# Kernel tuning notes

Hardware: AMD Instinct MI355X
Metric: run time of the kernel (lower is better)

Reference implementation:

```python
import jax, jax.numpy as jnp
import numpy as np

WINDOW = 9
REG_WEIGHT = 1.0


def _box_filter(x, k):
    """Sum over a k^3 box via three separable 1D ones-convs (== conv3d with ones kernel)."""
    pad = k // 2
    for ax in range(3):  # D, H, W spatial axes
        kshape = [1, 1, 1, 1, 1]
        kshape[2 + ax] = k
        kern = jnp.ones(kshape, x.dtype)
        padding = [(pad, pad) if i == ax else (0, 0) for i in range(3)]
        x = jax.lax.conv_general_dilated(
            x, kern, window_strides=(1, 1, 1), padding=padding,
            dimension_numbers=("NCDHW", "OIDHW", "NCDHW"))
    return x


def _ncc_loss(pred, target, k):
    win_size = jnp.asarray(float(k ** 3), pred.dtype)
    pred_sum = _box_filter(pred, k)
    target_sum = _box_filter(target, k)
    pred_sq_sum = _box_filter(pred * pred, k)
    target_sq_sum = _box_filter(target * target, k)
    pred_target_sum = _box_filter(pred * target, k)
    pred_mean = pred_sum / win_size
    target_mean = target_sum / win_size
    cross = (pred_target_sum - target_mean * pred_sum - pred_mean * target_sum
             + pred_mean * target_mean * win_size)
    pred_var = pred_sq_sum - 2.0 * pred_mean * pred_sum + pred_mean * pred_mean * win_size
    target_var = target_sq_sum - 2.0 * target_mean * target_sum + target_mean * target_mean * win_size
    pred_var = jnp.clip(pred_var, 0.0, None)
    target_var = jnp.clip(target_var, 0.0, None)
    cc = cross * cross / (pred_var * target_var + 0.001)
    cc = jnp.clip(cc, 0.0, 1.0)
    return 1.0 - jnp.mean(cc)


def _gradient_loss(flow):
    dy = jnp.abs(flow[:, :, 1:, :, :] - flow[:, :, :-1, :, :])
    dx = jnp.abs(flow[:, :, :, 1:, :] - flow[:, :, :, :-1, :])
    dz = jnp.abs(flow[:, :, :, :, 1:] - flow[:, :, :, :, :-1])
    return (jnp.mean(dy) + jnp.mean(dx) + jnp.mean(dz)) / 3.0


def setup_inputs() -> dict:
    key = jax.random.key(0)
    k1, k2, k3 = jax.random.split(key, 3)
    B, D, H, W = 2, 160, 160, 160
    moved = jax.random.uniform(k1, (B, 1, D, H, W), dtype=jnp.float32)
    fixed = jax.random.uniform(k2, (B, 1, D, H, W), dtype=jnp.float32)
    flow = jax.random.normal(k3, (B, 3, D, H, W), dtype=jnp.float32)
    return {"moved": moved, "fixed": fixed, "flow": flow}


def reference(moved, fixed, flow):
    sim_loss = _ncc_loss(moved, fixed, WINDOW)
    reg_loss = _gradient_loss(flow)
    total_loss = sim_loss + REG_WEIGHT * reg_loss
    return total_loss
```

## Files before the change

### kernel.cpp

```cpp
#include <hip/hip_runtime.h>

#define DD 160
#define HH 160
#define WW 160
#define VOL (DD * HH * WW)
#define PLANE (HH * WW)
#define NB 2
#define HT 16
#define HS (HT + 8)
#define LDW 164
#define DCH 20
#define NDCH (DD / DCH)
#define CPT 50
#define DREDBLK (CPT * NDCH)
#define GCHD 20
#define GBLK (NB * 3 * (DD / GCHD) * HH * (WW / 4) / 256)

typedef _Float16 h4 __attribute__((ext_vector_type(4)));
typedef _Float16 h2 __attribute__((ext_vector_type(2)));

__global__ __launch_bounds__(512, 4) void ncc_wh(const float* __restrict__ mv,
                                                 const float* __restrict__ fx,
                                                 _Float16* __restrict__ out) {
    __shared__ float wsum[5][HS][LDW];

    const int d   = blockIdx.y;
    const int b   = blockIdx.z;
    const int h0  = blockIdx.x * HT;
    const int tid = threadIdx.x;

    if (tid < 480) {
        const int r  = tid / 20;
        const int s  = tid - r * 20;
        const int h  = h0 - 4 + r;
        const int w0 = 8 * s;

        float vm[16], vf[16];
#pragma unroll
        for (int i = 0; i < 16; ++i) { vm[i] = 0.f; vf[i] = 0.f; }

        if ((unsigned)h < (unsigned)HH) {
            const float* rowm = mv + (size_t)b * VOL + ((size_t)d * HH + h) * WW;
            const float* rowf = fx + (size_t)b * VOL + ((size_t)d * HH + h) * WW;
#pragma unroll
            for (int j = 0; j < 4; ++j) {
                const int w4 = w0 - 4 + 4 * j;
                if (w4 >= 0 && w4 <= WW - 4) {
                    float4 m4 = *(const float4*)(rowm + w4);
                    float4 f4 = *(const float4*)(rowf + w4);
                    vm[4*j+0] = m4.x; vm[4*j+1] = m4.y; vm[4*j+2] = m4.z; vm[4*j+3] = m4.w;
                    vf[4*j+0] = f4.x; vf[4*j+1] = f4.y; vf[4*j+2] = f4.z; vf[4*j+3] = f4.w;
                } else {
#pragma unroll
                    for (int e = 0; e < 4; ++e) {
                        const int w = w4 + e;
                        if ((unsigned)w < (unsigned)WW) {
                            vm[4*j+e] = rowm[w];
                            vf[4*j+e] = rowf[w];
                        }
                    }
                }
            }
        }

        float o0[8], o1[8], o2[8], o3[8], o4[8];
        float sm = 0.f, sf = 0.f, smm = 0.f, sff = 0.f, smf = 0.f;
#pragma unroll
        for (int i = 0; i < 9; ++i) {
            float m = vm[i], f = vf[i];
            sm += m; sf += f;
            smm = fmaf(m, m, smm);
            sff = fmaf(f, f, sff);
            smf = fmaf(m, f, smf);
        }
        o0[0] = sm; o1[0] = sf; o2[0] = smm; o3[0] = sff; o4[0] = smf;
#pragma unroll
        for (int k = 1; k < 8; ++k) {
            float am = vm[k + 8], bm = vm[k - 1];
            float af = vf[k + 8], bf = vf[k - 1];
            sm  += am - bm;
            sf  += af - bf;
            smm += fmaf(am, am, -(bm * bm));
            sff += fmaf(af, af, -(bf * bf));
            smf += fmaf(am, af, -(bm * bf));
            o0[k] = sm; o1[k] = sf; o2[k] = smm; o3[k] = sff; o4[k] = smf;
        }
        *(float4*)&wsum[0][r][w0]     = *(float4*)&o0[0];
        *(float4*)&wsum[0][r][w0 + 4] = *(float4*)&o0[4];
        *(float4*)&wsum[1][r][w0]     = *(float4*)&o1[0];
        *(float4*)&wsum[1][r][w0 + 4] = *(float4*)&o1[4];
        *(float4*)&wsum[2][r][w0]     = *(float4*)&o2[0];
        *(float4*)&wsum[2][r][w0 + 4] = *(float4*)&o2[4];
        *(float4*)&wsum[3][r][w0]     = *(float4*)&o3[0];
        *(float4*)&wsum[3][r][w0 + 4] = *(float4*)&o3[4];
        *(float4*)&wsum[4][r][w0]     = *(float4*)&o4[0];
        *(float4*)&wsum[4][r][w0 + 4] = *(float4*)&o4[4];
    }
    __syncthreads();

    if (tid < 400) {
        const int f    = tid / 80;
        const int rem  = tid - f * 80;
        const int half = rem / 40;
        const int w    = 4 * (rem - half * 40);
        const int ro0  = 8 * half;

        float4 s9 = make_float4(0.f, 0.f, 0.f, 0.f);
#pragma unroll
        for (int t = 0; t < 9; ++t) {
            float4 v = *(const float4*)&wsum[f][ro0 + t][w];
            s9.x += v.x; s9.y += v.y; s9.z += v.z; s9.w += v.w;
        }
        _Float16* ob = out + (size_t)(b * 5 + f) * VOL
                           + ((size_t)d * HH + h0 + ro0) * WW + w;
        h4 o;
        o.x = (_Float16)s9.x; o.y = (_Float16)s9.y;
        o.z = (_Float16)s9.z; o.w = (_Float16)s9.w;
        *(h4*)ob = o;
#pragma unroll
        for (int ro = 1; ro < 8; ++ro) {
            float4 aa = *(const float4*)&wsum[f][ro0 + ro + 8][w];
            float4 bb = *(const float4*)&wsum[f][ro0 + ro - 1][w];
            s9.x += aa.x - bb.x; s9.y += aa.y - bb.y;
            s9.z += aa.z - bb.z; s9.w += aa.w - bb.w;
            o.x = (_Float16)s9.x; o.y = (_Float16)s9.y;
            o.z = (_Float16)s9.z; o.w = (_Float16)s9.w;
            *(h4*)(ob + (size_t)ro * WW) = o;
        }
    }
}

__global__ __launch_bounds__(256) void ncc_dred(const _Float16* __restrict__ fields,
                                                float* __restrict__ partial) {
    const int hw = (blockIdx.x * 256 + threadIdx.x) * 2;
    const int d0 = blockIdx.y * DCH;
    const _Float16* p0 = fields + (size_t)blockIdx.z * 5 * VOL + hw;

    float s0a = 0.f, s1a = 0.f, s2a = 0.f, s3a = 0.f, s4a = 0.f;
    float s0b = 0.f, s1b = 0.f, s2b = 0.f, s3b = 0.f, s4b = 0.f;
    {
        int lo = d0 - 4 > 0 ? d0 - 4 : 0;
        int hi = d0 + 4 < DD - 1 ? d0 + 4 : DD - 1;
        for (int dd = lo; dd <= hi; ++dd) {
            const _Float16* p = p0 + (size_t)dd * PLANE;
            h2 v0 = *(const h2*)(p + 0 * (size_t)VOL);
            h2 v1 = *(const h2*)(p + 1 * (size_t)VOL);
            h2 v2 = *(const h2*)(p + 2 * (size_t)VOL);
            h2 v3 = *(const h2*)(p + 3 * (size_t)VOL);
            h2 v4 = *(const h2*)(p + 4 * (size_t)VOL);
            s0a += (float)v0.x; s0b += (float)v0.y;
            s1a += (float)v1.x; s1b += (float)v1.y;
            s2a += (float)v2.x; s2b += (float)v2.y;
            s3a += (float)v3.x; s3b += (float)v3.y;
            s4a += (float)v4.x; s4b += (float)v4.y;
        }
    }

    float acc = 0.f;
    const float inv_win = 1.0f / 729.0f;
    for (int d = d0; d < d0 + DCH; ++d) {
        {
            float cross = fmaf(-(s0a * s1a), inv_win, s4a);
            float pv = fmaxf(fmaf(-(s0a * s0a), inv_win, s2a), 0.f);
            float tv = fmaxf(fmaf(-(s1a * s1a), inv_win, s3a), 0.f);
            float cc = cross * cross / (pv * tv + 0.001f);
            acc += fminf(fmaxf(cc, 0.f), 1.f);
        }
        {
            float cross = fmaf(-(s0b * s1b), inv_win, s4b);
            float pv = fmaxf(fmaf(-(s0b * s0b), inv_win, s2b), 0.f);
            float tv = fmaxf(fmaf(-(s1b * s1b), inv_win, s3b), 0.f);
            float cc = cross * cross / (pv * tv + 0.001f);
            acc += fminf(fmaxf(cc, 0.f), 1.f);
        }

        if (d + 1 < d0 + DCH) {
            if (d + 5 < DD) {
                const _Float16* p = p0 + (size_t)(d + 5) * PLANE;
                h2 v0 = *(const h2*)(p + 0 * (size_t)VOL);
                h2 v1 = *(const h2*)(p + 1 * (size_t)VOL);
                h2 v2 = *(const h2*)(p + 2 * (size_t)VOL);
                h2 v3 = *(const h2*)(p + 3 * (size_t)VOL);
                h2 v4 = *(const h2*)(p + 4 * (size_t)VOL);
                s0a += (float)v0.x; s0b += (float)v0.y;
                s1a += (float)v1.x; s1b += (float)v1.y;
                s2a += (float)v2.x; s2b += (float)v2.y;
                s3a += (float)v3.x; s3b += (float)v3.y;
                s4a += (float)v4.x; s4b += (float)v4.y;
            }
            if (d - 4 >= 0) {
                const _Float16* p = p0 + (size_t)(d - 4) * PLANE;
                h2 v0 = *(const h2*)(p + 0 * (size_t)VOL);
                h2 v1 = *(const h2*)(p + 1 * (size_t)VOL);
                h2 v2 = *(const h2*)(p + 2 * (size_t)VOL);
                h2 v3 = *(const h2*)(p + 3 * (size_t)VOL);
                h2 v4 = *(const h2*)(p + 4 * (size_t)VOL);
                s0a -= (float)v0.x; s0b -= (float)v0.y;
                s1a -= (float)v1.x; s1b -= (float)v1.y;
                s2a -= (float)v2.x; s2b -= (float)v2.y;
                s3a -= (float)v3.x; s3b -= (float)v3.y;
                s4a -= (float)v4.x; s4b -= (float)v4.y;
            }
        }
    }

    for (int o = 32; o > 0; o >>= 1) acc += __shfl_down(acc, o, 64);
    __shared__ float red[4];
    int lane = threadIdx.x & 63, wid = threadIdx.x >> 6;
    if (lane == 0) red[wid] = acc;
    __syncthreads();
    if (threadIdx.x == 0)
        partial[((size_t)blockIdx.z * NDCH + blockIdx.y) * CPT + blockIdx.x] =
            red[0] + red[1] + red[2] + red[3];
}

__global__ __launch_bounds__(256) void grad_red(const float* __restrict__ fl,
                                                float* __restrict__ partial) {
    const int gid = blockIdx.x * 256 + threadIdx.x;
    const int w4  = gid % 40;
    int t = gid / 40;
    const int h  = t % HH;  t /= HH;
    const int dc = t % (DD / GCHD); t /= (DD / GCHD);
    const int bc = t;
    const int d0 = dc * GCHD;
    const int w  = w4 * 4;

    const float* base = fl + (size_t)bc * VOL;
    float acc = 0.f;
    float4 v = *(const float4*)(base + ((size_t)d0 * HH + h) * WW + w);
    for (int d = d0; d < d0 + GCHD; ++d) {
        const float* pd = base + ((size_t)d * HH + h) * WW + w;
        float4 vn = v;
        if (d < DD - 1) {
            vn = *(const float4*)(pd + PLANE);
            acc += fabsf(vn.x - v.x) + fabsf(vn.y - v.y) +
                   fabsf(vn.z - v.z) + fabsf(vn.w - v.w);
        }
        if (h < HH - 1) {
            float4 vh = *(const float4*)(pd + WW);
            acc += fabsf(vh.x - v.x) + fabsf(vh.y - v.y) +
                   fabsf(vh.z - v.z) + fabsf(vh.w - v.w);
        }
        acc += fabsf(v.y - v.x) + fabsf(v.z - v.y) + fabsf(v.w - v.z);
        if (w < WW - 4) acc += fabsf(pd[4] - v.w);
        v = vn;
    }

    for (int o = 32; o > 0; o >>= 1) acc += __shfl_down(acc, o, 64);
    __shared__ float red[4];
    int lane = threadIdx.x & 63, wid = threadIdx.x >> 6;
    if (lane == 0) red[wid] = acc;
    __syncthreads();
    if (threadIdx.x == 0) partial[blockIdx.x] = red[0] + red[1] + red[2] + red[3];
}

__global__ __launch_bounds__(256) void finalize(const float* __restrict__ pcc, int ncc,
                                                const float* __restrict__ pg, int ng,
                                                float* __restrict__ out) {
    __shared__ float red[4];
    int lane = threadIdx.x & 63, wid = threadIdx.x >> 6;

    float a = 0.f;
    for (int i = threadIdx.x; i < ncc; i += 256) a += pcc[i];
    for (int o = 32; o > 0; o >>= 1) a += __shfl_down(a, o, 64);
    if (lane == 0) red[wid] = a;
    __syncthreads();
    float asum = red[0] + red[1] + red[2] + red[3];
    __syncthreads();

    float g = 0.f;
    for (int i = threadIdx.x; i < ng; i += 256) g += pg[i];
    for (int o = 32; o > 0; o >>= 1) g += __shfl_down(g, o, 64);
    if (lane == 0) red[wid] = g;
    __syncthreads();
    float gsum = red[0] + red[1] + red[2] + red[3];

    if (threadIdx.x == 0) {
        float sim = 1.0f - asum / 8192000.0f;
        float reg = gsum / 73267200.0f;
        out[0] = sim + reg;
    }
}

extern "C" void kernel_launch(void* const* d_in, const int* in_sizes, int n_in,
                              void* d_out, int out_size, void* d_ws, size_t ws_size,
                              hipStream_t stream) {
    const float* moved  = (const float*)d_in[0];
    const float* fixedp = (const float*)d_in[1];
    const float* flow   = (const float*)d_in[2];
    float* out = (float*)d_out;

    _Float16* fields = (_Float16*)d_ws;
    float* pcc = (float*)(fields + (size_t)NB * 5 * VOL);
    float* pg  = pcc + NB * DREDBLK;

    grad_red<<<GBLK, 256, 0, stream>>>(flow, pg);
    ncc_wh<<<dim3(HH / HT, DD, NB), 512, 0, stream>>>(moved, fixedp, fields);
    ncc_dred<<<dim3(CPT, NDCH, NB), 256, 0, stream>>>(fields, pcc);
    finalize<<<1, 256, 0, stream>>>(pcc, NB * DREDBLK, pg, GBLK, out);
}
```

Baseline: 97.65 us.

## Store W-pass sums as fp16 in LDS, widen H-pass to 8 columns, halve D chunk

The intermediate W-direction window sums in shared memory are now stored as fp16 instead of fp32, halving LDS footprint so occupancy can rise (launch bound min blocks raised to 6). The H-pass threads now process 8 columns by 4 rows with 16-byte fp16 loads and stores instead of 4 columns by 8 rows. The D-reduction chunk size is halved, doubling blocks in that kernel. Rounding intermediate sums to fp16 before the H sum adds precision loss, especially for squared sums.

```diff
diff --git a/kernel.cpp b/kernel.cpp
--- a/kernel.cpp
+++ b/kernel.cpp
@@ -8,21 +8,21 @@
 #define NB 2
 #define HT 16
 #define HS (HT + 8)
-#define LDW 164
-#define DCH 20
+#define LDWH 168
+#define DCH 10
 #define NDCH (DD / DCH)
 #define CPT 50
 #define DREDBLK (CPT * NDCH)
 #define GCHD 20
 #define GBLK (NB * 3 * (DD / GCHD) * HH * (WW / 4) / 256)
 
-typedef _Float16 h4 __attribute__((ext_vector_type(4)));
+typedef _Float16 h8 __attribute__((ext_vector_type(8)));
 typedef _Float16 h2 __attribute__((ext_vector_type(2)));
 
-__global__ __launch_bounds__(512, 4) void ncc_wh(const float* __restrict__ mv,
+__global__ __launch_bounds__(512, 6) void ncc_wh(const float* __restrict__ mv,
                                                  const float* __restrict__ fx,
                                                  _Float16* __restrict__ out) {
-    __shared__ float wsum[5][HS][LDW];
+    __shared__ _Float16 wsum[5][HS][LDWH];
 
     const int d   = blockIdx.y;
     const int b   = blockIdx.z;
@@ -85,47 +85,48 @@
             smf += fmaf(am, af, -(bm * bf));
             o0[k] = sm; o1[k] = sf; o2[k] = smm; o3[k] = sff; o4[k] = smf;
         }
-        *(float4*)&wsum[0][r][w0]     = *(float4*)&o0[0];
-        *(float4*)&wsum[0][r][w0 + 4] = *(float4*)&o0[4];
-        *(float4*)&wsum[1][r][w0]     = *(float4*)&o1[0];
-        *(float4*)&wsum[1][r][w0 + 4] = *(float4*)&o1[4];
-        *(float4*)&wsum[2][r][w0]     = *(float4*)&o2[0];
-        *(float4*)&wsum[2][r][w0 + 4] = *(float4*)&o2[4];
-        *(float4*)&wsum[3][r][w0]     = *(float4*)&o3[0];
-        *(float4*)&wsum[3][r][w0 + 4] = *(float4*)&o3[4];
-        *(float4*)&wsum[4][r][w0]     = *(float4*)&o4[0];
-        *(float4*)&wsum[4][r][w0 + 4] = *(float4*)&o4[4];
+#define PACK_STORE(fi, arr) {                                   \
+            h8 t_;                                              \
+            _Pragma("unroll")                                   \
+            for (int j_ = 0; j_ < 8; ++j_) t_[j_] = (_Float16)arr[j_]; \
+            *(h8*)&wsum[fi][r][w0] = t_; }
+        PACK_STORE(0, o0) PACK_STORE(1, o1) PACK_STORE(2, o2)
+        PACK_STORE(3, o3) PACK_STORE(4, o4)
+#undef PACK_STORE
     }
     __syncthreads();
 
     if (tid < 400) {
-        const int f    = tid / 80;
-        const int rem  = tid - f * 80;
-        const int half = rem / 40;
-        const int w    = 4 * (rem - half * 40);
-        const int ro0  = 8 * half;
-
-        float4 s9 = make_float4(0.f, 0.f, 0.f, 0.f);
+        const int f   = tid / 80;
+        const int rem = tid - f * 80;
+        const int q   = rem / 20;
+        const int w   = 8 * (rem - q * 20);
+        const int ro0 = 4 * q;
+
+        float sa[8];
+#pragma unroll
+        for (int j = 0; j < 8; ++j) sa[j] = 0.f;
 #pragma unroll
         for (int t = 0; t < 9; ++t) {
-            float4 v = *(const float4*)&wsum[f][ro0 + t][w];
-            s9.x += v.x; s9.y += v.y; s9.z += v.z; s9.w += v.w;
+            h8 v = *(const h8*)&wsum[f][ro0 + t][w];
+#pragma unroll
+            for (int j = 0; j < 8; ++j) sa[j] += (float)v[j];
         }
         _Float16* ob = out + (size_t)(b * 5 + f) * VOL
                            + ((size_t)d * HH + h0 + ro0) * WW + w;
-        h4 o;
-        o.x = (_Float16)s9.x; o.y = (_Float16)s9.y;
-        o.z = (_Float16)s9.z; o.w = (_Float16)s9.w;
-        *(h4*)ob = o;
-#pragma unroll
-        for (int ro = 1; ro < 8; ++ro) {
-            float4 aa = *(const float4*)&wsum[f][ro0 + ro + 8][w];
-            float4 bb = *(const float4*)&wsum[f][ro0 + ro - 1][w];
-            s9.x += aa.x - bb.x; s9.y += aa.y - bb.y;
-            s9.z += aa.z - bb.z; s9.w += aa.w - bb.w;
-            o.x = (_Float16)s9.x; o.y = (_Float16)s9.y;
-            o.z = (_Float16)s9.z; o.w = (_Float16)s9.w;
-            *(h4*)(ob + (size_t)ro * WW) = o;
+        h8 o;
+#pragma unroll
+        for (int j = 0; j < 8; ++j) o[j] = (_Float16)sa[j];
+        *(h8*)ob = o;
+#pragma unroll
+        for (int ro = 1; ro < 4; ++ro) {
+            h8 va = *(const h8*)&wsum[f][ro0 + ro + 8][w];
+            h8 vb = *(const h8*)&wsum[f][ro0 + ro - 1][w];
+#pragma unroll
+            for (int j = 0; j < 8; ++j) sa[j] += (float)va[j] - (float)vb[j];
+#pragma unroll
+            for (int j = 0; j < 8; ++j) o[j] = (_Float16)sa[j];
+            *(h8*)(ob + (size_t)ro * WW) = o;
         }
     }
 }
```

After: 97.34 us. Within noise of the previous version (-0.3%).
